# Optimization experiments

Hardware: AMD Instinct MI355X
Metric: run time of the kernel (lower is better)

The kernel has to match this reference:

```python
import jax, jax.numpy as jnp
import numpy as np

B, L, D, H = 1, 1024, 768, 12
h = D // H  # 64
EPS = 1e-5
ALPHA = 0.01  # leaky relu slope


def setup_inputs() -> dict:
    key = jax.random.key(0)
    ks = jax.random.split(key, 10)
    s = 0.02
    f32 = jnp.float32
    return {
        "x": jax.random.normal(ks[0], (B, L, D), f32),
        "filters": jax.random.normal(ks[1], (L, h), f32) * s,  # spectral filters [L, h]
        "wq_w": jax.random.normal(ks[2], (D, D), f32) * s,
        "wq_b": jnp.zeros((D,), f32),
        "wk_w": jax.random.normal(ks[3], (D, D), f32) * s,
        "wk_b": jnp.zeros((D,), f32),
        "wv_w": jax.random.normal(ks[4], (D, D), f32) * s,
        "wv_b": jnp.zeros((D,), f32),
        "wo_w": jax.random.normal(ks[5], (D, D), f32) * s,
        "wo_b": jnp.zeros((D,), f32),
        "wg_w": jax.random.normal(ks[6], (h * h, 1), f32) * s,
        "wg_b": jnp.zeros((1,), f32),
        "qk_scale": jnp.ones((1, H, 1), f32) + jax.random.normal(ks[7], (1, H, 1), f32) * 0.02,
        "kv_scale": jnp.ones((1, H, 1, 1, 1), f32) + jax.random.normal(ks[8], (1, H, 1, 1, 1), f32) * 0.02,
    }


def _causal_fft_conv(f, u):
    """Per-head-channel causal FFT convolution. f: [L,h], u: [B,H,L,h] -> [B,H,L,h]."""
    n = 2 * L  # >= L + L - 1 for linear (full) convolution
    Ff = jnp.fft.rfft(f, n=n, axis=0)            # [n//2+1, h]
    Uf = jnp.fft.rfft(u, n=n, axis=2)            # [B,H,n//2+1,h]
    y = jnp.fft.irfft(Uf * Ff[None, None], n=n, axis=2)
    return y[:, :, :L, :]


def _l2norm(t):
    # matches F.normalize(dim=-1): x / max(||x||, 1e-12)
    nrm = jnp.sqrt(jnp.sum(t * t, axis=-1, keepdims=True))
    return t / jnp.maximum(nrm, 1e-12)


def _combine(a, b):
    """Associative combine: (m, s, n, Z, g) running-max / exp-sum / exp-weighted-v / outer-product / gate-sum."""
    m_x, s_x, n_x, Z_x, g_x = a
    m_y, s_y, n_y, Z_y, g_y = b
    m = jnp.maximum(m_x, m_y)
    ex = jnp.exp(m_x - m)
    ey = jnp.exp(m_y - m)
    return (m,
            s_x * ex + s_y * ey,
            n_x * ex[..., None] + n_y * ey[..., None],
            Z_x + Z_y,
            g_x + g_y)


def reference(x, filters, wq_w, wq_b, wk_w, wk_b, wv_w, wv_b, wo_w, wo_b,
              wg_w, wg_b, qk_scale, kv_scale):
    # split heads: [B,H,L,h]
    bhld = x.reshape(B, L, H, h).transpose(0, 2, 1, 3)
    # spectral filtering (tensordot_conv): per-channel causal conv with filters
    xt = _causal_fft_conv(filters, bhld)                       # [B,H,L,h]
    xt = xt.transpose(0, 2, 1, 3).reshape(B, L, D)             # [B,L,D]

    q = (xt @ wq_w + wq_b).reshape(B, L, H, h).transpose(0, 2, 1, 3)
    k = (xt @ wk_w + wk_b).reshape(B, L, H, h).transpose(0, 2, 1, 3)
    v = (xt @ wv_w + wv_b).reshape(B, L, H, h).transpose(0, 2, 1, 3)
    q, k, v = _l2norm(q), _l2norm(k), _l2norm(v)

    sim = jnp.einsum('bhld,bhld->bhl', q, k) * qk_scale         # [B,H,L]
    # Z[b,h,s,p,n] = v[b,h,s,p] * k[b,h,s,n]
    Z = jnp.einsum('bhsn,bhsp->bhspn', k, v) * kv_scale         # [B,H,L,h,h]

    gate_logits = Z.reshape(B, H, L, h * h) @ wg_w + wg_b       # [B,H,L,1]
    gl = jnp.where(gate_logits > 0, gate_logits, ALPHA * gate_logits)
    gates = (gl * gl + EPS)[..., 0]                             # [B,H,L]
    gated_Z = Z * gates[..., None, None]

    leaves = (sim, jnp.ones_like(sim), v, gated_Z, gates)
    m_s, s_s, n_s, Z_s, g_s = jax.lax.associative_scan(_combine, leaves, axis=2)

    linear_attn = n_s / (s_s[..., None] + EPS)                  # [B,H,L,h]
    softmax_w = jnp.exp(sim - m_s) / (s_s + EPS)                # [B,H,L]
    Hm = Z_s / (g_s[..., None, None] + EPS)                     # [B,H,L,h,h]
    ctx = jnp.einsum('bhtp,bhtpn->bhtn', q, Hm)                 # [B,H,L,h]
    qla = linear_attn
    lerp = ctx + (qla - ctx) * softmax_w[..., None]

    y = lerp.transpose(0, 2, 1, 3).reshape(B, L, D)
    return y @ wo_w + wo_b
```

## Files before the change

### kernel.cpp

```cpp
#include <hip/hip_runtime.h>
#include <hip/hip_bf16.h>

constexpr int LS = 1024;
constexpr int DM = 768;
constexpr int NH = 12;
constexpr int HD = 64;
constexpr float EPSF = 1e-5f;
constexpr float ALPHAF = 0.01f;

constexpr int SG = 16;
constexpr int NTL = LS / SG;
constexpr int WSZ = DM * DM;

typedef unsigned short u16;
typedef __attribute__((ext_vector_type(8))) short bf16x8;
typedef __attribute__((ext_vector_type(8))) unsigned short u16x8;
typedef __attribute__((ext_vector_type(4))) float f32x4;

__device__ __forceinline__ u16 f2b(float f) {
  unsigned u = __float_as_uint(f);
  u += 0x7FFFu + ((u >> 16) & 1u);
  return (u16)(u >> 16);
}

__device__ __forceinline__ void gld16(const u16* g, void* l) {
  __builtin_amdgcn_global_load_lds(
      (const __attribute__((address_space(1))) void*)g,
      (__attribute__((address_space(3))) void*)l, 16, 0, 0);
}

__global__ __launch_bounds__(256) void txw_kernel(const float* __restrict__ wq,
                                                  const float* __restrict__ wk,
                                                  const float* __restrict__ wv,
                                                  const float* __restrict__ wo,
                                                  u16* __restrict__ wT) {
  const int z = blockIdx.z;
  const float* src = (z == 0) ? wq : (z == 1) ? wk : (z == 2) ? wv : wo;
  u16* dst = wT + (size_t)z * WSZ;
  const int kb = blockIdx.x * 64, nb = blockIdx.y * 64;
  const int t = threadIdx.x;
  __shared__ float T[64][65];
#pragma unroll
  for (int rep = 0; rep < 4; ++rep) {
    const int r = rep * 16 + (t >> 4);
    const int c4 = (t & 15) * 4;
    const float4 v4 = *(const float4*)(src + (size_t)(kb + r) * DM + nb + c4);
    T[r][c4] = v4.x; T[r][c4 + 1] = v4.y; T[r][c4 + 2] = v4.z; T[r][c4 + 3] = v4.w;
  }
  __syncthreads();
#pragma unroll
  for (int rep = 0; rep < 4; ++rep) {
    const int n = rep * 16 + (t >> 4);
    const int k4 = (t & 15) * 4;
    ushort4 o;
    o.x = f2b(T[k4 + 0][n]); o.y = f2b(T[k4 + 1][n]);
    o.z = f2b(T[k4 + 2][n]); o.w = f2b(T[k4 + 3][n]);
    *(ushort4*)(dst + (size_t)(nb + n) * DM + kb + k4) = o;
  }
}

__global__ __launch_bounds__(256) void conv_kernel(const float* __restrict__ x,
                                                   const float* __restrict__ f,
                                                   float* __restrict__ p0,
                                                   float* __restrict__ p1,
                                                   float* __restrict__ p2,
                                                   float* __restrict__ p3) {
  const int i    = blockIdx.x;
  const int head = blockIdx.y;
  const int par  = blockIdx.z;
  const int tid  = threadIdx.x;
  const int c    = tid & 63;
  const int sg   = tid >> 6;
  const int tbase = i * 64;
  const int l0w   = tbase + sg * 16;
  float* __restrict__ xt_p = (par == 0) ? p0 : (par == 1) ? p1 : (par == 2) ? p2 : p3;

  __shared__ float4 Xs2[28][64];

  {
    const float4 z4 = make_float4(0.f, 0.f, 0.f, 0.f);
#pragma unroll
    for (int k = 0; k < 3; ++k) {
      const int lin = k * 256 + tid;
      const int g   = lin >> 6;
      const int cc  = lin & 63;
      const int grp = (g < 4) ? g : (16 + g);
      Xs2[grp][cc] = z4;
    }
  }

  float acc[16];
#pragma unroll
  for (int t = 0; t < 16; ++t) acc[t] = 0.f;

  const float* xg   = x + head * HD + c;
  const float* fcol = f + c;

  for (int j = par; j <= i; j += 4) {
    const int sbase = j * 64;
    const int b0 = (j < i) ? (tbase - sbase - 64) : 0;
#pragma unroll
    for (int k = 0; k < 4; ++k) {
      const int m  = sg + 4 * k;
      const int ss = 4 * m;
      float4 v4;
      v4.x = xg[(sbase + ss + 0) * DM];
      v4.y = xg[(sbase + ss + 1) * DM];
      v4.z = xg[(sbase + ss + 2) * DM];
      v4.w = xg[(sbase + ss + 3) * DM];
      Xs2[4 + m][c] = v4;
    }
    __syncthreads();

    const int dstart = (j < i) ? (b0 + sg * 16) : 0;
    const int nsteps = (j < i) ? 5 : (sg + 1);
    for (int k = 0; k < nsteps; ++k) {
      const int d0    = dstart + 16 * k;
      const int rbase = l0w - d0 - sbase;
      float fr[16];
#pragma unroll
      for (int m = 0; m < 16; ++m) fr[m] = fcol[(d0 + m) * HD];
      float xw[32];
      const int xgb = rbase >> 2;
#pragma unroll
      for (int m = 0; m < 8; ++m) {
        const float4 v4 = Xs2[xgb + m][c];
        xw[4 * m + 0] = v4.x; xw[4 * m + 1] = v4.y;
        xw[4 * m + 2] = v4.z; xw[4 * m + 3] = v4.w;
      }
#pragma unroll
      for (int li = 0; li < 16; ++li)
#pragma unroll
        for (int dd = 0; dd < 16; ++dd)
          acc[li] = fmaf(fr[dd], xw[li - dd + 16], acc[li]);
    }
    __syncthreads();
  }

#pragma unroll
  for (int li = 0; li < 16; ++li)
    xt_p[(size_t)(l0w + li) * DM + head * HD + c] = acc[li];
}

__global__ __launch_bounds__(256) void pack_xt(const float* __restrict__ a,
                                               const float* __restrict__ b,
                                               const float* __restrict__ cc,
                                               const float* __restrict__ d,
                                               u16* __restrict__ xtb) {
  const size_t i = ((size_t)blockIdx.x * 256 + threadIdx.x) * 8;
  u16x8 o;
#pragma unroll
  for (int h = 0; h < 2; ++h) {
    const float4 a4 = *(const float4*)(a + i + h * 4);
    const float4 b4 = *(const float4*)(b + i + h * 4);
    const float4 c4 = *(const float4*)(cc + i + h * 4);
    const float4 d4 = *(const float4*)(d + i + h * 4);
    o[h * 4 + 0] = f2b(a4.x + b4.x + c4.x + d4.x);
    o[h * 4 + 1] = f2b(a4.y + b4.y + c4.y + d4.y);
    o[h * 4 + 2] = f2b(a4.z + b4.z + c4.z + d4.z);
    o[h * 4 + 3] = f2b(a4.w + b4.w + c4.w + d4.w);
  }
  *(u16x8*)(xtb + i) = o;
}

__global__ __launch_bounds__(256) void qkv_mfma(const u16* __restrict__ xtb,
                                                const u16* __restrict__ wT,
                                                const float* __restrict__ bq,
                                                const float* __restrict__ bk,
                                                const float* __restrict__ bv,
                                                float* __restrict__ qo,
                                                float* __restrict__ ko,
                                                float* __restrict__ vo) {
  const int b = blockIdx.x;
  const int xcd = b & 7, j = b >> 3;
  const int unit = xcd * 9 + (j >> 3), sub = j & 7;
  const int z = unit / 24, rem = unit % 24;
  const int ct = rem >> 1, rt = (rem & 1) * 8 + sub;

  __shared__ u16 As[64 * 64];
  __shared__ u16 Bs[64 * 64];

  const int tid = threadIdx.x, w = tid >> 6, l = tid & 63;
  const int wr = w >> 1, wc = w & 1;

  const int srow1 = tid >> 3, sc16 = tid & 7;
  const int c16L1 = sc16 ^ (srow1 & 7);
  const int srow2 = srow1 + 32;
  const int c16L2 = sc16 ^ (srow2 & 7);

  const u16* wz = wT + (size_t)z * WSZ;
  const u16* Ag1 = xtb + (size_t)(rt * 64 + srow1) * DM + c16L1 * 8;
  const u16* Ag2 = xtb + (size_t)(rt * 64 + srow2) * DM + c16L2 * 8;
  const u16* Bg1 = wz + (size_t)(ct * 64 + srow1) * DM + c16L1 * 8;
  const u16* Bg2 = wz + (size_t)(ct * 64 + srow2) * DM + c16L2 * 8;

  char* lA = (char*)As + w * 1024;
  char* lB = (char*)Bs + w * 1024;

  f32x4 acc[2][2] = {};
  for (int kb = 0; kb < DM; kb += 64) {
    gld16(Ag1 + kb, lA);
    gld16(Ag2 + kb, lA + 4096);
    gld16(Bg1 + kb, lB);
    gld16(Bg2 + kb, lB + 4096);
    __syncthreads();
#pragma unroll
    for (int kk = 0; kk < 2; ++kk) {
      bf16x8 a[2], bb[2];
#pragma unroll
      for (int ar = 0; ar < 2; ++ar) {
        const int row = wr * 32 + ar * 16 + (l & 15);
        const int c16 = ((kk << 2) + (l >> 4)) ^ (row & 7);
        a[ar] = *(const bf16x8*)((char*)As + row * 128 + c16 * 16);
      }
#pragma unroll
      for (int bc = 0; bc < 2; ++bc) {
        const int col = wc * 32 + bc * 16 + (l & 15);
        const int c16 = ((kk << 2) + (l >> 4)) ^ (col & 7);
        bb[bc] = *(const bf16x8*)((char*)Bs + col * 128 + c16 * 16);
      }
#pragma unroll
      for (int ar = 0; ar < 2; ++ar)
#pragma unroll
        for (int bc = 0; bc < 2; ++bc)
          acc[ar][bc] = __builtin_amdgcn_mfma_f32_16x16x32_bf16(
              a[ar], bb[bc], acc[ar][bc], 0, 0, 0);
    }
    __syncthreads();
  }

  const float* bias = (z == 0) ? bq : (z == 1) ? bk : bv;
  float* out = (z == 0) ? qo : (z == 1) ? ko : vo;
  const int rbase = rt * 64 + wr * 32 + ((l >> 4) << 2);
  const int cb = wc * 32 + (l & 15);
#pragma unroll
  for (int ar = 0; ar < 2; ++ar)
#pragma unroll
    for (int bc = 0; bc < 2; ++bc) {
      const int col = cb + bc * 16;
      const float bbv = bias[ct * 64 + col];
#pragma unroll
      for (int r = 0; r < 4; ++r)
        out[((size_t)ct * LS + rbase + ar * 16 + r) * HD + col] =
            acc[ar][bc][r] + bbv;
    }
}

__global__ __launch_bounds__(256) void out_mfma(const u16* __restrict__ lerpb,
                                                const u16* __restrict__ woT,
                                                const float* __restrict__ bias,
                                                float* __restrict__ out) {
  const int b = blockIdx.x;
  const int xcd = b & 7, j = b >> 3;
  const int unit = xcd * 3 + (j >> 3), sub = j & 7;
  const int ct = unit >> 1, rt = (unit & 1) * 8 + sub;

  __shared__ u16 As[64 * 64];
  __shared__ u16 Bs[64 * 64];

  const int tid = threadIdx.x, w = tid >> 6, l = tid & 63;
  const int wr = w >> 1, wc = w & 1;

  const int srow1 = tid >> 3, sc16 = tid & 7;
  const int c16L1 = sc16 ^ (srow1 & 7);
  const int srow2 = srow1 + 32;
  const int c16L2 = sc16 ^ (srow2 & 7);

  const u16* Ag1 = lerpb + (size_t)(rt * 64 + srow1) * DM + c16L1 * 8;
  const u16* Ag2 = lerpb + (size_t)(rt * 64 + srow2) * DM + c16L2 * 8;
  const u16* Bg1 = woT + (size_t)(ct * 64 + srow1) * DM + c16L1 * 8;
  const u16* Bg2 = woT + (size_t)(ct * 64 + srow2) * DM + c16L2 * 8;

  char* lA = (char*)As + w * 1024;
  char* lB = (char*)Bs + w * 1024;

  f32x4 acc[2][2] = {};
  for (int kb = 0; kb < DM; kb += 64) {
    gld16(Ag1 + kb, lA);
    gld16(Ag2 + kb, lA + 4096);
    gld16(Bg1 + kb, lB);
    gld16(Bg2 + kb, lB + 4096);
    __syncthreads();
#pragma unroll
    for (int kk = 0; kk < 2; ++kk) {
      bf16x8 a[2], bb[2];
#pragma unroll
      for (int ar = 0; ar < 2; ++ar) {
        const int row = wr * 32 + ar * 16 + (l & 15);
        const int c16 = ((kk << 2) + (l >> 4)) ^ (row & 7);
        a[ar] = *(const bf16x8*)((char*)As + row * 128 + c16 * 16);
      }
#pragma unroll
      for (int bc = 0; bc < 2; ++bc) {
        const int col = wc * 32 + bc * 16 + (l & 15);
        const int c16 = ((kk << 2) + (l >> 4)) ^ (col & 7);
        bb[bc] = *(const bf16x8*)((char*)Bs + col * 128 + c16 * 16);
      }
#pragma unroll
      for (int ar = 0; ar < 2; ++ar)
#pragma unroll
        for (int bc = 0; bc < 2; ++bc)
          acc[ar][bc] = __builtin_amdgcn_mfma_f32_16x16x32_bf16(
              a[ar], bb[bc], acc[ar][bc], 0, 0, 0);
    }
    __syncthreads();
  }

  const int rbase = rt * 64 + wr * 32 + ((l >> 4) << 2);
  const int cb = wc * 32 + (l & 15);
#pragma unroll
  for (int ar = 0; ar < 2; ++ar)
#pragma unroll
    for (int bc = 0; bc < 2; ++bc) {
      const int col = ct * 64 + cb + bc * 16;
      const float bbv = bias[col];
#pragma unroll
      for (int r = 0; r < 4; ++r)
        out[(size_t)(rbase + ar * 16 + r) * DM + col] = acc[ar][bc][r] + bbv;
    }
}

__global__ void norm_sim_gate(float* __restrict__ q, float* __restrict__ k, float* __restrict__ v,
                              const float* __restrict__ wg, const float* __restrict__ wgb,
                              const float* __restrict__ qk_scale, const float* __restrict__ kv_scale,
                              float* __restrict__ sim, float* __restrict__ gates) {
  const int w = threadIdx.x >> 6, lane = threadIdx.x & 63;
  const int l = blockIdx.x * 4 + w;
  const int head = blockIdx.y;
  const size_t idx = ((size_t)head * LS + l) * HD + lane;
  float qv = q[idx], kv = k[idx], vv = v[idx];

  auto red = [](float x) {
#pragma unroll
    for (int o = 32; o; o >>= 1) x += __shfl_xor(x, o);
    return x;
  };
  const float qn = fmaxf(sqrtf(red(qv * qv)), 1e-12f);
  const float kn = fmaxf(sqrtf(red(kv * kv)), 1e-12f);
  const float vn = fmaxf(sqrtf(red(vv * vv)), 1e-12f);
  qv /= qn; kv /= kn; vv /= vn;
  q[idx] = qv; k[idx] = kv; v[idx] = vv;

  const float s = red(qv * kv) * qk_scale[head];

  __shared__ float vs[4][64];
  vs[w][lane] = vv;
  __syncthreads();
  float t = 0.f;
#pragma unroll 8
  for (int p = 0; p < 64; ++p) t = fmaf(vs[w][p], wg[p * 64 + lane], t);
  float gl = red(t * kv) * kv_scale[head] + wgb[0];
  gl = gl > 0.f ? gl : ALPHAF * gl;
  const float g = gl * gl + EPSF;
  if (lane == 0) {
    sim[head * LS + l] = s;
    gates[head * LS + l] = g;
  }
}

__global__ void scan_kernel(const float* __restrict__ sim, const float* __restrict__ gates,
                            float* __restrict__ m_s, float* __restrict__ Sraw,
                            float* __restrict__ g_s) {
  const int head = blockIdx.x, t = threadIdx.x;
  __shared__ float bm[1024], bs[1024], bg[1024];
  const float sv = sim[head * LS + t];
  float m = sv, S = expf(sv), g = gates[head * LS + t];
  bm[t] = m; bs[t] = S; bg[t] = g;
  __syncthreads();
  for (int off = 1; off < 1024; off <<= 1) {
    float om = -1e30f, os = 0.f, og = 0.f;
    if (t >= off) { om = bm[t - off]; os = bs[t - off]; og = bg[t - off]; }
    __syncthreads();
    m = fmaxf(m, om); S += os; g += og;
    bm[t] = m; bs[t] = S; bg[t] = g;
    __syncthreads();
  }
  m_s[head * LS + t] = m;
  Sraw[head * LS + t] = S;
  g_s[head * LS + t] = g;
}

__global__ __launch_bounds__(256) void state_kernel(const float* __restrict__ k,
                                                    const float* __restrict__ v,
                                                    const float* __restrict__ sim,
                                                    const float* __restrict__ gates,
                                                    float* __restrict__ states,
                                                    float* __restrict__ nes) {
  const int j = blockIdx.x, head = blockIdx.y;
  const int s0 = j * SG;
  const int tid = threadIdx.x;
  __shared__ alignas(16) float Vs[SG][68];
  __shared__ alignas(16) float Kg[SG][68];
  __shared__ float Es[SG];

  const int r = tid >> 4, c = (tid & 15) * 4;
  const float* kh = k + ((size_t)head * LS + s0) * HD;
  const float* vh = v + ((size_t)head * LS + s0) * HD;
  const float g = gates[head * LS + s0 + r];
  *(float4*)&Vs[r][c] = *(const float4*)(vh + r * HD + c);
  float4 k4 = *(const float4*)(kh + r * HD + c);
  k4.x *= g; k4.y *= g; k4.z *= g; k4.w *= g;
  *(float4*)&Kg[r][c] = k4;
  if (tid < SG) Es[tid] = expf(sim[head * LS + s0 + tid]);
  __syncthreads();

  const int p0 = (tid >> 4) * 4, n0 = (tid & 15) * 4;
  float acc[4][4] = {};
  for (int s = 0; s < SG; ++s) {
    const float4 ra = *(const float4*)&Vs[s][p0];
    const float4 rb = *(const float4*)&Kg[s][n0];
    const float av[4] = {ra.x, ra.y, ra.z, ra.w};
    const float bv[4] = {rb.x, rb.y, rb.z, rb.w};
#pragma unroll
    for (int i = 0; i < 4; ++i)
#pragma unroll
      for (int jj = 0; jj < 4; ++jj)
        acc[i][jj] = fmaf(av[i], bv[jj], acc[i][jj]);
  }
  float* Sout = states + (size_t)(head * NTL + j) * 4096;
#pragma unroll
  for (int i = 0; i < 4; ++i)
    *(float4*)&Sout[(p0 + i) * 64 + n0] =
        make_float4(acc[i][0], acc[i][1], acc[i][2], acc[i][3]);

  if (tid < HD) {
    float ne = 0.f;
    for (int s = 0; s < SG; ++s) ne = fmaf(Es[s], Vs[s][tid], ne);
    nes[(size_t)(head * NTL + j) * HD + tid] = ne;
  }
}

__global__ __launch_bounds__(256) void prefix_kernel(float* __restrict__ states,
                                                     float* __restrict__ nes) {
  const int head = blockIdx.x, chunk = blockIdx.y;
  const int tid = threadIdx.x;
  const int off = chunk * 1024 + tid * 4;
  float4 acc = make_float4(0.f, 0.f, 0.f, 0.f);
  float* base = states + (size_t)head * NTL * 4096 + off;
#pragma unroll 4
  for (int j = 0; j < NTL; ++j) {
    float4* p = (float4*)(base + (size_t)j * 4096);
    const float4 sv = *p;
    *p = acc;
    acc.x += sv.x; acc.y += sv.y; acc.z += sv.z; acc.w += sv.w;
  }
  if (chunk == 0 && tid < HD) {
    float a = 0.f;
    float* nb = nes + (size_t)head * NTL * HD + tid;
#pragma unroll 4
    for (int j = 0; j < NTL; ++j) {
      float* p = nb + (size_t)j * HD;
      const float t = *p;
      *p = a;
      a += t;
    }
  }
}

__global__ __launch_bounds__(256) void apply_kernel(const float* __restrict__ q,
                                                    const float* __restrict__ k,
                                                    const float* __restrict__ v,
                                                    const float* __restrict__ sim,
                                                    const float* __restrict__ gates,
                                                    const float* __restrict__ m_s,
                                                    const float* __restrict__ Sraw,
                                                    const float* __restrict__ g_s,
                                                    const float* __restrict__ states,
                                                    const float* __restrict__ nes,
                                                    const float* __restrict__ kv_scale,
                                                    u16* __restrict__ lerpb) {
  const int bt = blockIdx.x, head = blockIdx.y;
  const int t0 = bt * SG;
  const int tid = threadIdx.x;
  __shared__ alignas(16) float Ps[64][68];
  __shared__ alignas(16) float Qs[SG][68];
  __shared__ alignas(16) float Vs[SG][68];
  __shared__ alignas(16) float Ks[SG][68];
  __shared__ alignas(16) float NEp[64];
  __shared__ float Ag[SG][SG + 1];
  __shared__ float Es[SG], Gs[SG];

  const float* Pg = states + (size_t)(head * NTL + bt) * 4096;
#pragma unroll
  for (int rep = 0; rep < 4; ++rep) {
    const int lin = rep * 1024 + tid * 4;
    *(float4*)&Ps[lin >> 6][lin & 63] = *(const float4*)(Pg + lin);
  }
  {
    const int r = tid >> 4, c = (tid & 15) * 4;
    const size_t rowbase = ((size_t)head * LS + t0 + r) * HD;
    *(float4*)&Qs[r][c] = *(const float4*)(q + rowbase + c);
    *(float4*)&Ks[r][c] = *(const float4*)(k + rowbase + c);
    *(float4*)&Vs[r][c] = *(const float4*)(v + rowbase + c);
  }
  if (tid < SG) {
    Es[tid] = expf(sim[head * LS + t0 + tid]);
    Gs[tid] = gates[head * LS + t0 + tid];
  }
  if (tid < HD) NEp[tid] = nes[(size_t)(head * NTL + bt) * HD + tid];
  __syncthreads();

  {
    const int t = tid >> 4, s = tid & 15;
    float a = 0.f;
    if (s <= t) {
#pragma unroll
      for (int p = 0; p < 64; p += 4) {
        const float4 q4 = *(const float4*)&Qs[t][p];
        const float4 v4 = *(const float4*)&Vs[s][p];
        a = fmaf(q4.x, v4.x, a); a = fmaf(q4.y, v4.y, a);
        a = fmaf(q4.z, v4.z, a); a = fmaf(q4.w, v4.w, a);
      }
      a *= Gs[s];
    }
    Ag[t][s] = a;
  }
  __syncthreads();

  const int r = tid >> 4, c0 = (tid & 15) * 4;
  float4 O = make_float4(0.f, 0.f, 0.f, 0.f);
#pragma unroll 8
  for (int p = 0; p < 64; ++p) {
    const float qv = Qs[r][p];
    const float4 p4 = *(const float4*)&Ps[p][c0];
    O.x = fmaf(qv, p4.x, O.x); O.y = fmaf(qv, p4.y, O.y);
    O.z = fmaf(qv, p4.z, O.z); O.w = fmaf(qv, p4.w, O.w);
  }
  float4 Nn = *(const float4*)&NEp[c0];
  for (int s = 0; s <= r; ++s) {
    const float ag = Ag[r][s];
    const float es = Es[s];
    const float4 k4 = *(const float4*)&Ks[s][c0];
    const float4 v4 = *(const float4*)&Vs[s][c0];
    O.x = fmaf(ag, k4.x, O.x); O.y = fmaf(ag, k4.y, O.y);
    O.z = fmaf(ag, k4.z, O.z); O.w = fmaf(ag, k4.w, O.w);
    Nn.x = fmaf(es, v4.x, Nn.x); Nn.y = fmaf(es, v4.y, Nn.y);
    Nn.z = fmaf(es, v4.z, Nn.z); Nn.w = fmaf(es, v4.w, Nn.w);
  }

  const int t = t0 + r;
  const float m  = m_s[head * LS + t];
  const float em = expf(-m);
  const float ss = Sraw[head * LS + t] * em;
  const float inv = 1.f / (ss + EPSF);
  const float sw  = expf(sim[head * LS + t] - m) * inv;
  const float gi  = kv_scale[head] / (g_s[head * LS + t] + EPSF);
  const float ei  = em * inv;
  float rx, ry, rz, rw;
  { const float cx = O.x * gi, la = Nn.x * ei; rx = cx + (la - cx) * sw; }
  { const float cx = O.y * gi, la = Nn.y * ei; ry = cx + (la - cx) * sw; }
  { const float cx = O.z * gi, la = Nn.z * ei; rz = cx + (la - cx) * sw; }
  { const float cx = O.w * gi, la = Nn.w * ei; rw = cx + (la - cx) * sw; }
  ushort4 ob;
  ob.x = f2b(rx); ob.y = f2b(ry); ob.z = f2b(rz); ob.w = f2b(rw);
  *(ushort4*)&lerpb[(size_t)t * DM + head * HD + c0] = ob;
}

extern "C" void kernel_launch(void* const* d_in, const int* in_sizes, int n_in,
                              void* d_out, int out_size, void* d_ws, size_t ws_size,
                              hipStream_t stream) {
  (void)in_sizes; (void)n_in; (void)out_size; (void)ws_size;
  const float* x        = (const float*)d_in[0];
  const float* filters  = (const float*)d_in[1];
  const float* wq_w     = (const float*)d_in[2];
  const float* wq_b     = (const float*)d_in[3];
  const float* wk_w     = (const float*)d_in[4];
  const float* wk_b     = (const float*)d_in[5];
  const float* wv_w     = (const float*)d_in[6];
  const float* wv_b     = (const float*)d_in[7];
  const float* wo_w     = (const float*)d_in[8];
  const float* wo_b     = (const float*)d_in[9];
  const float* wg_w     = (const float*)d_in[10];
  const float* wg_b     = (const float*)d_in[11];
  const float* qk_scale = (const float*)d_in[12];
  const float* kv_scale = (const float*)d_in[13];

  float* ws = (float*)d_ws;
  const size_t NT = (size_t)LS * DM;
  float* xt_a  = ws;
  float* xt_b  = ws + NT;
  float* q     = ws + 2 * NT;
  float* k     = ws + 3 * NT;
  float* v     = ws + 4 * NT;
  float* sim   = ws + 5 * NT;
  float* gates = sim + NH * LS;
  float* m_s   = gates + NH * LS;
  float* Sraw  = m_s + NH * LS;
  float* g_s   = Sraw + NH * LS;
  float* states = g_s + NH * LS;
  float* nes    = states + (size_t)NH * NTL * 4096;
  u16*   xtb    = (u16*)(nes + (size_t)NH * NTL * HD);
  u16*   wT     = xtb + NT;
  u16*   lerpb  = (u16*)xt_a;

  txw_kernel<<<dim3(DM / 64, DM / 64, 4), 256, 0, stream>>>(wq_w, wk_w, wv_w, wo_w, wT);
  conv_kernel<<<dim3(LS / 64, NH, 4), 256, 0, stream>>>(x, filters, xt_a, xt_b, q, k);
  pack_xt<<<dim3(NT / 2048), 256, 0, stream>>>(xt_a, xt_b, q, k, xtb);
  qkv_mfma<<<dim3(576), 256, 0, stream>>>(xtb, wT, wq_b, wk_b, wv_b, q, k, v);
  norm_sim_gate<<<dim3(LS / 4, NH), 256, 0, stream>>>(
      q, k, v, wg_w, wg_b, qk_scale, kv_scale, sim, gates);
  scan_kernel<<<dim3(NH), 1024, 0, stream>>>(sim, gates, m_s, Sraw, g_s);
  state_kernel<<<dim3(NTL, NH), 256, 0, stream>>>(k, v, sim, gates, states, nes);
  prefix_kernel<<<dim3(NH, 4), 256, 0, stream>>>(states, nes);
  apply_kernel<<<dim3(NTL, NH), 256, 0, stream>>>(
      q, k, v, sim, gates, m_s, Sraw, g_s, states, nes, kv_scale, lerpb);
  out_mfma<<<dim3(192), 256, 0, stream>>>(
      lerpb, wT + 3 * (size_t)WSZ, wo_b, (float*)d_out);
}
```

Measured before the change: 108.5 us.

## Merge weight transpose into conv kernel and split conv causal loop eight ways

Folds the weight transpose/bf16 conversion into the causal convolution kernel as extra blocks of a single launch, removing one kernel launch and letting the transpose overlap with conv work. The conv's partial sums are now split across 8 parallel partitions instead of 4, which gives more blocks and a shorter per-block loop for the heavily loaded late tiles. In exchange, pack_xt must read and reduce 8 fp32 partial buffers instead of 4, and extra workspace is used for them.

```diff
diff --git a/kernel.cpp b/kernel.cpp
--- a/kernel.cpp
+++ b/kernel.cpp
@@ -11,6 +11,7 @@
 constexpr int SG = 16;
 constexpr int NTL = LS / SG;
 constexpr int WSZ = DM * DM;
+constexpr int NPAR = 8;
 
 typedef unsigned short u16;
 typedef __attribute__((ext_vector_type(8))) short bf16x8;
@@ -29,53 +30,51 @@
       (__attribute__((address_space(3))) void*)l, 16, 0, 0);
 }
 
-__global__ __launch_bounds__(256) void txw_kernel(const float* __restrict__ wq,
-                                                  const float* __restrict__ wk,
-                                                  const float* __restrict__ wv,
-                                                  const float* __restrict__ wo,
-                                                  u16* __restrict__ wT) {
-  const int z = blockIdx.z;
-  const float* src = (z == 0) ? wq : (z == 1) ? wk : (z == 2) ? wv : wo;
-  u16* dst = wT + (size_t)z * WSZ;
-  const int kb = blockIdx.x * 64, nb = blockIdx.y * 64;
-  const int t = threadIdx.x;
-  __shared__ float T[64][65];
-#pragma unroll
-  for (int rep = 0; rep < 4; ++rep) {
-    const int r = rep * 16 + (t >> 4);
-    const int c4 = (t & 15) * 4;
-    const float4 v4 = *(const float4*)(src + (size_t)(kb + r) * DM + nb + c4);
-    T[r][c4] = v4.x; T[r][c4 + 1] = v4.y; T[r][c4 + 2] = v4.z; T[r][c4 + 3] = v4.w;
-  }
-  __syncthreads();
-#pragma unroll
-  for (int rep = 0; rep < 4; ++rep) {
-    const int n = rep * 16 + (t >> 4);
-    const int k4 = (t & 15) * 4;
-    ushort4 o;
-    o.x = f2b(T[k4 + 0][n]); o.y = f2b(T[k4 + 1][n]);
-    o.z = f2b(T[k4 + 2][n]); o.w = f2b(T[k4 + 3][n]);
-    *(ushort4*)(dst + (size_t)(nb + n) * DM + kb + k4) = o;
-  }
-}
-
-__global__ __launch_bounds__(256) void conv_kernel(const float* __restrict__ x,
-                                                   const float* __restrict__ f,
-                                                   float* __restrict__ p0,
-                                                   float* __restrict__ p1,
-                                                   float* __restrict__ p2,
-                                                   float* __restrict__ p3) {
-  const int i    = blockIdx.x;
-  const int head = blockIdx.y;
-  const int par  = blockIdx.z;
-  const int tid  = threadIdx.x;
+__global__ __launch_bounds__(256) void conv_txw_kernel(
+    const float* __restrict__ x, const float* __restrict__ f,
+    const float* __restrict__ wq, const float* __restrict__ wk,
+    const float* __restrict__ wv, const float* __restrict__ wo,
+    u16* __restrict__ wT, float* __restrict__ pbase) {
+  extern __shared__ char smem[];
+  const int b = blockIdx.x;
+  const int tid = threadIdx.x;
+
+  if (b >= 1536) {
+    const int b2 = b - 1536;
+    const int kb = (b2 % 12) * 64, nb = ((b2 / 12) % 12) * 64, z = b2 / 144;
+    const float* src = (z == 0) ? wq : (z == 1) ? wk : (z == 2) ? wv : wo;
+    u16* dst = wT + (size_t)z * WSZ;
+    float (*T)[65] = (float(*)[65])smem;
+#pragma unroll
+    for (int rep = 0; rep < 4; ++rep) {
+      const int r = rep * 16 + (tid >> 4);
+      const int c4 = (tid & 15) * 4;
+      const float4 v4 = *(const float4*)(src + (size_t)(kb + r) * DM + nb + c4);
+      T[r][c4] = v4.x; T[r][c4 + 1] = v4.y; T[r][c4 + 2] = v4.z; T[r][c4 + 3] = v4.w;
+    }
+    __syncthreads();
+#pragma unroll
+    for (int rep = 0; rep < 4; ++rep) {
+      const int n = rep * 16 + (tid >> 4);
+      const int k4 = (tid & 15) * 4;
+      ushort4 o;
+      o.x = f2b(T[k4 + 0][n]); o.y = f2b(T[k4 + 1][n]);
+      o.z = f2b(T[k4 + 2][n]); o.w = f2b(T[k4 + 3][n]);
+      *(ushort4*)(dst + (size_t)(nb + n) * DM + kb + k4) = o;
+    }
+    return;
+  }
+
+  const int i    = b & 15;
+  const int head = (b >> 4) % 12;
+  const int par  = b / 192;
   const int c    = tid & 63;
   const int sg   = tid >> 6;
   const int tbase = i * 64;
   const int l0w   = tbase + sg * 16;
-  float* __restrict__ xt_p = (par == 0) ? p0 : (par == 1) ? p1 : (par == 2) ? p2 : p3;
-
-  __shared__ float4 Xs2[28][64];
+  float* __restrict__ xt_p = pbase + (size_t)par * LS * DM;
+
+  float4 (*Xs2)[64] = (float4(*)[64])smem;
 
   {
     const float4 z4 = make_float4(0.f, 0.f, 0.f, 0.f);
@@ -96,7 +95,7 @@
   const float* xg   = x + head * HD + c;
   const float* fcol = f + c;
 
-  for (int j = par; j <= i; j += 4) {
+  for (int j = par; j <= i; j += NPAR) {
     const int sbase = j * 64;
     const int b0 = (j < i) ? (tbase - sbase - 64) : 0;
 #pragma unroll
@@ -142,23 +141,21 @@
     xt_p[(size_t)(l0w + li) * DM + head * HD + c] = acc[li];
 }
 
-__global__ __launch_bounds__(256) void pack_xt(const float* __restrict__ a,
-                                               const float* __restrict__ b,
-                                               const float* __restrict__ cc,
-                                               const float* __restrict__ d,
+__global__ __launch_bounds__(256) void pack_xt(const float* __restrict__ pbase,
                                                u16* __restrict__ xtb) {
+  const size_t NT = (size_t)LS * DM;
   const size_t i = ((size_t)blockIdx.x * 256 + threadIdx.x) * 8;
   u16x8 o;
 #pragma unroll
   for (int h = 0; h < 2; ++h) {
-    const float4 a4 = *(const float4*)(a + i + h * 4);
-    const float4 b4 = *(const float4*)(b + i + h * 4);
-    const float4 c4 = *(const float4*)(cc + i + h * 4);
-    const float4 d4 = *(const float4*)(d + i + h * 4);
-    o[h * 4 + 0] = f2b(a4.x + b4.x + c4.x + d4.x);
-    o[h * 4 + 1] = f2b(a4.y + b4.y + c4.y + d4.y);
-    o[h * 4 + 2] = f2b(a4.z + b4.z + c4.z + d4.z);
-    o[h * 4 + 3] = f2b(a4.w + b4.w + c4.w + d4.w);
+    float4 s = make_float4(0.f, 0.f, 0.f, 0.f);
+#pragma unroll
+    for (int p = 0; p < NPAR; ++p) {
+      const float4 v4 = *(const float4*)(pbase + p * NT + i + h * 4);
+      s.x += v4.x; s.y += v4.y; s.z += v4.z; s.w += v4.w;
+    }
+    o[h * 4 + 0] = f2b(s.x); o[h * 4 + 1] = f2b(s.y);
+    o[h * 4 + 2] = f2b(s.z); o[h * 4 + 3] = f2b(s.w);
   }
   *(u16x8*)(xtb + i) = o;
 }
@@ -577,12 +574,10 @@
 
   float* ws = (float*)d_ws;
   const size_t NT = (size_t)LS * DM;
-  float* xt_a  = ws;
-  float* xt_b  = ws + NT;
-  float* q     = ws + 2 * NT;
-  float* k     = ws + 3 * NT;
-  float* v     = ws + 4 * NT;
-  float* sim   = ws + 5 * NT;
+  float* q     = ws;
+  float* k     = ws + NT;
+  float* v     = ws + 2 * NT;
+  float* sim   = ws + 3 * NT;
   float* gates = sim + NH * LS;
   float* m_s   = gates + NH * LS;
   float* Sraw  = m_s + NH * LS;
@@ -591,11 +586,12 @@
   float* nes    = states + (size_t)NH * NTL * 4096;
   u16*   xtb    = (u16*)(nes + (size_t)NH * NTL * HD);
   u16*   wT     = xtb + NT;
-  u16*   lerpb  = (u16*)xt_a;
-
-  txw_kernel<<<dim3(DM / 64, DM / 64, 4), 256, 0, stream>>>(wq_w, wk_w, wv_w, wo_w, wT);
-  conv_kernel<<<dim3(LS / 64, NH, 4), 256, 0, stream>>>(x, filters, xt_a, xt_b, q, k);
-  pack_xt<<<dim3(NT / 2048), 256, 0, stream>>>(xt_a, xt_b, q, k, xtb);
+  u16*   lerpb  = wT + 4 * (size_t)WSZ;
+  float* pbase  = (float*)(lerpb + NT);
+
+  conv_txw_kernel<<<dim3(2112), 256, 28672, stream>>>(
+      x, filters, wq_w, wk_w, wv_w, wo_w, wT, pbase);
+  pack_xt<<<dim3(NT / 2048), 256, 0, stream>>>(pbase, xtb);
   qkv_mfma<<<dim3(576), 256, 0, stream>>>(xtb, wT, wq_b, wk_b, wv_b, q, k, v);
   norm_sim_gate<<<dim3(LS / 4, NH), 256, 0, stream>>>(
       q, k, v, wg_w, wg_b, qk_scale, kv_scale, sim, gates);
```

Result: faster. 102.5 us (-5.5%).
